# Kernel tuning notes

Hardware: AMD Instinct MI355X
Metric: run time of the kernel (lower is better)

## Reference

```python
import jax, jax.numpy as jnp
import numpy as np

IN_FEATURES = 4096
OUT_FEATURES = 4096
RANK = 16
N_BITS = 4
SCALING = 0.01
QMIN = -(2 ** (N_BITS - 1))      # -8
QMAX = 2 ** (N_BITS - 1) - 1     #  7
EPS = 1e-8


@jax.custom_vjp
def ste_quant(x, scale):
    """Fake-quantize with straight-through estimator (zero_point = 0)."""
    q = jnp.clip(jnp.round(x / scale), QMIN, QMAX)
    return q * scale


def _ste_fwd(x, scale):
    return ste_quant(x, scale), (x, scale)


def _ste_bwd(res, g):
    x, scale = res
    q = x / scale
    mask = ((q >= QMIN) & (q <= QMAX)).astype(g.dtype)
    # Torch STE returns grad only for input; scale gets no gradient.
    gs = jnp.zeros(scale.shape, dtype=g.dtype)
    return (g * mask, gs)


ste_quant.defvjp(_ste_fwd, _ste_bwd)


def setup_inputs() -> dict:
    key = jax.random.key(0)
    ks = jax.random.split(key, 4)
    x = jax.random.normal(ks[0], (4, 2048, IN_FEATURES), dtype=jnp.float32)
    pretrained_weight = 0.1 * jax.random.normal(ks[1], (OUT_FEATURES, IN_FEATURES), dtype=jnp.float32)
    lora_A = np.sqrt(2.0 / RANK) * jax.random.normal(ks[2], (RANK, IN_FEATURES), dtype=jnp.float32)
    # Original inits lora_B to zeros; use small random values so the LoRA path is non-degenerate.
    lora_B = 0.01 * jax.random.normal(ks[3], (OUT_FEATURES, RANK), dtype=jnp.float32)
    # Mirror initialize_scales(): per-channel 99th-percentile |w| / 2^(n_bits-1).
    weight_max = jnp.quantile(jnp.abs(pretrained_weight), 0.99, axis=1)
    weight_scale = weight_max / (2 ** (N_BITS - 1))
    activation_scale = jnp.ones((1,), dtype=jnp.float32)
    bias = jnp.zeros((OUT_FEATURES,), dtype=jnp.float32)
    return {
        "x": x,
        "pretrained_weight": pretrained_weight,
        "lora_A": lora_A,
        "lora_B": lora_B,
        "weight_scale": weight_scale,
        "activation_scale": activation_scale,
        "bias": bias,
    }


def reference(x, pretrained_weight, lora_A, lora_B, weight_scale, activation_scale, bias):
    # LoRA merge: [out, in]
    merged = pretrained_weight + SCALING * (lora_B @ lora_A)
    wsc = jnp.maximum(jnp.abs(weight_scale), EPS)      # [out]
    asc = jnp.maximum(jnp.abs(activation_scale), EPS)  # [1]
    # Per-output-channel fake quant of the weight (vectorized over the torch loop).
    w_q = ste_quant(merged, wsc[:, None])              # [out, in]
    x_q = ste_quant(x, asc)                            # [b, s, in]
    # F.linear: x_q @ w_q^T + bias
    return jnp.einsum("bsi,oi->bso", x_q, w_q) + bias
```

## Files before the change

kernel.cpp:

```cpp
#include <hip/hip_runtime.h>
#include <cstdint>
#include <cstddef>

#define IN_F 4096
#define OUT_F 4096
#define RANKK 16
#define EPSQ 1e-8f
#define LSCALE 0.01f

typedef __attribute__((ext_vector_type(4))) int i32x4;
typedef __attribute__((ext_vector_type(16))) int i32x16;

__device__ __forceinline__ float quantf(float v, float s) {
    float q = rintf(v / s);
    return fminf(7.f, fmaxf(-8.f, q));
}

__global__ __launch_bounds__(256) void qx_kernel(const float* __restrict__ x,
                                                 const float* __restrict__ ascale,
                                                 int8_t* __restrict__ qx) {
    const float asc = fmaxf(fabsf(ascale[0]), EPSQ);
    const int i = blockIdx.x * 256 + threadIdx.x;
    float4 v = ((const float4*)x)[i];
    union { int8_t b[4]; int w; } u;
    u.b[0] = (int8_t)(int)quantf(v.x, asc);
    u.b[1] = (int8_t)(int)quantf(v.y, asc);
    u.b[2] = (int8_t)(int)quantf(v.z, asc);
    u.b[3] = (int8_t)(int)quantf(v.w, asc);
    ((int*)qx)[i] = u.w;
}

__global__ __launch_bounds__(256) void qw_kernel(const float* __restrict__ W,
                                                 const float* __restrict__ lA,
                                                 const float* __restrict__ lB,
                                                 const float* __restrict__ wscale,
                                                 int8_t* __restrict__ qw) {
    __shared__ float Ablk[RANKK][256];
    __shared__ float Bblk[64][RANKK];
    const int tid = threadIdx.x;
    const int i0 = blockIdx.x * 256;
    const int o0 = blockIdx.y * 64;

#pragma unroll
    for (int r = 0; r < RANKK; ++r)
        Ablk[r][tid] = lA[r * IN_F + i0 + tid];
    for (int j = tid; j < 64 * RANKK; j += 256)
        Bblk[j >> 4][j & 15] = lB[(size_t)(o0 + (j >> 4)) * RANKK + (j & 15)];
    __syncthreads();

    const int i = i0 + tid;
#pragma unroll 4
    for (int o = 0; o < 64; ++o) {
        float s = 0.f;
#pragma unroll
        for (int r = 0; r < RANKK; ++r) s += Bblk[o][r] * Ablk[r][tid];
        float merged = W[(size_t)(o0 + o) * IN_F + i] + LSCALE * s;
        float wsc = fmaxf(fabsf(wscale[o0 + o]), EPSQ);
        qw[(size_t)(o0 + o) * IN_F + i] = (int8_t)(int)quantf(merged, wsc);
    }
}

constexpr int BM = 256, BN = 256, BK = 128, KD = 4096, NT = KD / BK;

__device__ __forceinline__ void gll16(const int8_t* g, const int8_t* l) {
    __builtin_amdgcn_global_load_lds(
        (const __attribute__((address_space(1))) void*)g,
        (__attribute__((address_space(3))) void*)l, 16, 0, 0);
}

__global__ __launch_bounds__(512, 2) void gemm_i8_kernel(
        const int8_t* __restrict__ qx, const int8_t* __restrict__ qw,
        const float* __restrict__ wscale, const float* __restrict__ ascale,
        const float* __restrict__ bias, float* __restrict__ out) {
    __shared__ __attribute__((aligned(16))) int8_t As[2][BM * BK];
    __shared__ __attribute__((aligned(16))) int8_t Bs[2][BN * BK];

    const int tid  = threadIdx.x;
    const int lane = tid & 63;
    const int wave = tid >> 6;
    const int hi   = lane >> 5;

    const int bid  = blockIdx.x;
    const int swz  = (bid & 7) * 64 + (bid >> 3);
    const int m_tile = (swz >> 4) * BM;
    const int n_tile = (swz & 15) * BN;

    const int wm = (wave >> 1) * 64;
    const int wn = (wave & 1) * 128;

    int src[4];
#pragma unroll
    for (int is = 0; is < 4; ++is) {
        int p = is * 512 + tid;
        int m = p >> 3;
        src[is] = m * KD + (((p & 7) ^ (m & 7)) << 4);
    }
    const int lds_u = wave * 1024;

    int aB[2], aH[2], bB[4], bH[4];
#pragma unroll
    for (int mi = 0; mi < 2; ++mi) {
        const int ra = wm + mi * 32 + (lane & 31);
        aB[mi] = ra * BK;
        aH[mi] = ra & 7;
    }
#pragma unroll
    for (int ni = 0; ni < 4; ++ni) {
        const int rb = wn + ni * 32 + (lane & 31);
        bB[ni] = rb * BK;
        bH[ni] = rb & 7;
    }

    const int8_t* Ab = qx + (size_t)m_tile * KD;
    const int8_t* Bb = qw + (size_t)n_tile * KD;

    i32x16 acc[2][4];
#pragma unroll
    for (int mi = 0; mi < 2; ++mi)
#pragma unroll
        for (int ni = 0; ni < 4; ++ni) acc[mi][ni] = (i32x16)(0);

#pragma unroll
    for (int is = 0; is < 4; ++is)
        gll16(Ab + src[is], &As[0][is * 8192 + lds_u]);
#pragma unroll
    for (int is = 0; is < 4; ++is)
        gll16(Bb + src[is], &Bs[0][is * 8192 + lds_u]);
    __syncthreads();

    for (int t = 0; t < NT; ++t) {
        const int buf = t & 1;
        if (t + 1 < NT) {
            const int k1 = (t + 1) * BK;
            int8_t* dA = (int8_t*)As[buf ^ 1];
            int8_t* dB = (int8_t*)Bs[buf ^ 1];
#pragma unroll
            for (int is = 0; is < 4; ++is)
                gll16(Ab + k1 + src[is], dA + is * 8192 + lds_u);
#pragma unroll
            for (int is = 0; is < 4; ++is)
                gll16(Bb + k1 + src[is], dB + is * 8192 + lds_u);
        }
        const int8_t* Asb = As[buf];
        const int8_t* Bsb = Bs[buf];
#pragma unroll
        for (int kk = 0; kk < 4; ++kk) {
            const int q = kk * 2 + hi;
            i32x4 af[2], bf[4];
#pragma unroll
            for (int mi = 0; mi < 2; ++mi)
                af[mi] = *(const i32x4*)(Asb + aB[mi] + ((q ^ aH[mi]) << 4));
#pragma unroll
            for (int ni = 0; ni < 4; ++ni)
                bf[ni] = *(const i32x4*)(Bsb + bB[ni] + ((q ^ bH[ni]) << 4));
#pragma unroll
            for (int mi = 0; mi < 2; ++mi)
#pragma unroll
                for (int ni = 0; ni < 4; ++ni)
                    acc[mi][ni] = __builtin_amdgcn_mfma_i32_32x32x32_i8(
                        af[mi], bf[ni], acc[mi][ni], 0, 0, 0);
        }
        if (t + 1 < NT) __syncthreads();
    }

    const float asc = fmaxf(fabsf(ascale[0]), EPSQ);
#pragma unroll
    for (int ni = 0; ni < 4; ++ni) {
        const int n  = n_tile + wn + ni * 32 + (lane & 31);
        const float sc = asc * fmaxf(fabsf(wscale[n]), EPSQ);
        const float bb = bias[n];
#pragma unroll
        for (int mi = 0; mi < 2; ++mi) {
            const int rbase = m_tile + wm + mi * 32 + 4 * hi;
#pragma unroll
            for (int r = 0; r < 16; ++r) {
                const int row = rbase + (r & 3) + 8 * (r >> 2);
                out[(size_t)row * OUT_F + n] = sc * (float)acc[mi][ni][r] + bb;
            }
        }
    }
}

extern "C" void kernel_launch(void* const* d_in, const int* in_sizes, int n_in,
                              void* d_out, int out_size, void* d_ws, size_t ws_size,
                              hipStream_t stream) {
    const float* x      = (const float*)d_in[0];
    const float* W      = (const float*)d_in[1];
    const float* lA     = (const float*)d_in[2];
    const float* lB     = (const float*)d_in[3];
    const float* wscale = (const float*)d_in[4];
    const float* ascale = (const float*)d_in[5];
    const float* bias   = (const float*)d_in[6];
    float* out = (float*)d_out;

    const int M = in_sizes[0] / IN_F;
    int8_t* qx = (int8_t*)d_ws;
    int8_t* qw = qx + (size_t)M * IN_F;

    qx_kernel<<<(in_sizes[0] / 4 + 255) / 256, 256, 0, stream>>>(x, ascale, qx);
    qw_kernel<<<dim3(IN_F / 256, OUT_F / 64), 256, 0, stream>>>(W, lA, lB, wscale, qw);
    gemm_i8_kernel<<<dim3((M / BM) * (OUT_F / BN)), 512, 0, stream>>>(
        qx, qw, wscale, ascale, bias, out);
}
```

Measured before the change: 437.7 us.

## Shrink int8 GEMM tiles to 128x256x64 with 256 threads and explicit vmcnt waits

Reduces the GEMM block tile to 128x256 with a K step of 64, cuts the workgroup to 4 waves, and reworks the LDS XOR swizzle to match 64-byte rows. The __syncthreads calls are replaced with explicit s_waitcnt vmcnt and s_barrier so the next tile's global-to-LDS loads stay in flight while the current tile computes. MFMA sections also get raised wave priority via s_setprio. The aim is higher occupancy (more blocks, smaller LDS footprint) and less time stalled at barriers, at the cost of less data reuse per block and a hand-tuned vmcnt count that relies on the exact load order.

Result: no change. 445.0 us (+1.7%).

```diff
diff --git a/kernel.cpp b/kernel.cpp
--- a/kernel.cpp
+++ b/kernel.cpp
@@ -60,7 +60,7 @@
     }
 }
 
-constexpr int BM = 256, BN = 256, BK = 128, KD = 4096, NT = KD / BK;
+constexpr int BM = 128, BN = 256, BK = 64, KD = 4096, NT = KD / BK;
 
 __device__ __forceinline__ void gll16(const int8_t* g, const int8_t* l) {
     __builtin_amdgcn_global_load_lds(
@@ -68,7 +68,7 @@
         (__attribute__((address_space(3))) void*)l, 16, 0, 0);
 }
 
-__global__ __launch_bounds__(512, 2) void gemm_i8_kernel(
+__global__ __launch_bounds__(256, 2) void gemm_i8_kernel(
         const int8_t* __restrict__ qx, const int8_t* __restrict__ qw,
         const float* __restrict__ wscale, const float* __restrict__ ascale,
         const float* __restrict__ bias, float* __restrict__ out) {
@@ -81,19 +81,23 @@
     const int hi   = lane >> 5;
 
     const int bid  = blockIdx.x;
-    const int swz  = (bid & 7) * 64 + (bid >> 3);
+    const int swz  = (bid & 7) * 128 + (bid >> 3);
     const int m_tile = (swz >> 4) * BM;
     const int n_tile = (swz & 15) * BN;
 
     const int wm = (wave >> 1) * 64;
     const int wn = (wave & 1) * 128;
 
-    int src[4];
+    int srcA[2], srcB[4];
+#pragma unroll
+    for (int is = 0; is < 2; ++is) {
+        int p = is * 256 + tid;
+        srcA[is] = (p >> 2) * KD + ((((p & 3) ^ ((p >> 3) & 3))) << 4);
+    }
 #pragma unroll
     for (int is = 0; is < 4; ++is) {
-        int p = is * 512 + tid;
-        int m = p >> 3;
-        src[is] = m * KD + (((p & 7) ^ (m & 7)) << 4);
+        int p = is * 256 + tid;
+        srcB[is] = (p >> 2) * KD + ((((p & 3) ^ ((p >> 3) & 3))) << 4);
     }
     const int lds_u = wave * 1024;
 
@@ -102,13 +106,13 @@
     for (int mi = 0; mi < 2; ++mi) {
         const int ra = wm + mi * 32 + (lane & 31);
         aB[mi] = ra * BK;
-        aH[mi] = ra & 7;
+        aH[mi] = (ra >> 1) & 3;
     }
 #pragma unroll
     for (int ni = 0; ni < 4; ++ni) {
         const int rb = wn + ni * 32 + (lane & 31);
         bB[ni] = rb * BK;
-        bH[ni] = rb & 7;
+        bH[ni] = (rb >> 1) & 3;
     }
 
     const int8_t* Ab = qx + (size_t)m_tile * KD;
@@ -121,12 +125,11 @@
         for (int ni = 0; ni < 4; ++ni) acc[mi][ni] = (i32x16)(0);
 
 #pragma unroll
+    for (int is = 0; is < 2; ++is)
+        gll16(Ab + srcA[is], &As[0][is * 4096 + lds_u]);
+#pragma unroll
     for (int is = 0; is < 4; ++is)
-        gll16(Ab + src[is], &As[0][is * 8192 + lds_u]);
-#pragma unroll
-    for (int is = 0; is < 4; ++is)
-        gll16(Bb + src[is], &Bs[0][is * 8192 + lds_u]);
-    __syncthreads();
+        gll16(Bb + srcB[is], &Bs[0][is * 4096 + lds_u]);
 
     for (int t = 0; t < NT; ++t) {
         const int buf = t & 1;
@@ -135,16 +138,21 @@
             int8_t* dA = (int8_t*)As[buf ^ 1];
             int8_t* dB = (int8_t*)Bs[buf ^ 1];
 #pragma unroll
+            for (int is = 0; is < 2; ++is)
+                gll16(Ab + k1 + srcA[is], dA + is * 4096 + lds_u);
+#pragma unroll
             for (int is = 0; is < 4; ++is)
-                gll16(Ab + k1 + src[is], dA + is * 8192 + lds_u);
-#pragma unroll
-            for (int is = 0; is < 4; ++is)
-                gll16(Bb + k1 + src[is], dB + is * 8192 + lds_u);
+                gll16(Bb + k1 + srcB[is], dB + is * 4096 + lds_u);
+            asm volatile("s_waitcnt vmcnt(6)" ::: "memory");
+        } else {
+            asm volatile("s_waitcnt vmcnt(0)" ::: "memory");
         }
+        asm volatile("s_barrier" ::: "memory");
+
         const int8_t* Asb = As[buf];
         const int8_t* Bsb = Bs[buf];
 #pragma unroll
-        for (int kk = 0; kk < 4; ++kk) {
+        for (int kk = 0; kk < 2; ++kk) {
             const int q = kk * 2 + hi;
             i32x4 af[2], bf[4];
 #pragma unroll
@@ -153,14 +161,16 @@
 #pragma unroll
             for (int ni = 0; ni < 4; ++ni)
                 bf[ni] = *(const i32x4*)(Bsb + bB[ni] + ((q ^ bH[ni]) << 4));
+            __builtin_amdgcn_s_setprio(1);
 #pragma unroll
             for (int mi = 0; mi < 2; ++mi)
 #pragma unroll
                 for (int ni = 0; ni < 4; ++ni)
                     acc[mi][ni] = __builtin_amdgcn_mfma_i32_32x32x32_i8(
                         af[mi], bf[ni], acc[mi][ni], 0, 0, 0);
+            __builtin_amdgcn_s_setprio(0);
         }
-        if (t + 1 < NT) __syncthreads();
+        asm volatile("s_barrier" ::: "memory");
     }
 
     const float asc = fmaxf(fabsf(ascale[0]), EPSQ);
@@ -199,6 +209,6 @@
 
     qx_kernel<<<(in_sizes[0] / 4 + 255) / 256, 256, 0, stream>>>(x, ascale, qx);
     qw_kernel<<<dim3(IN_F / 256, OUT_F / 64), 256, 0, stream>>>(W, lA, lB, wscale, qw);
-    gemm_i8_kernel<<<dim3((M / BM) * (OUT_F / BN)), 512, 0, stream>>>(
+    gemm_i8_kernel<<<dim3((M / BM) * (OUT_F / BN)), 256, 0, stream>>>(
         qx, qw, wscale, ascale, bias, out);
 }
```
